# Optimization experiments

Hardware: AMD Instinct MI355X
Metric: run time of the kernel (lower is better)

## Reference

```python
import jax, jax.numpy as jnp
import numpy as np

B, T, I, H, O = 256, 512, 64, 512, 1


def _lstm_layer(x, Wih, Whh, bih, bhh):
    # x: [B, T, in]; Wih: [4H, in]; Whh: [4H, H]
    # Precompute input contribution for all timesteps (big GEMM, no recurrence).
    xg = jnp.einsum('bti,gi->btg', x, Wih) + bih + bhh  # [B, T, 4H]
    h0 = jnp.zeros((x.shape[0], Whh.shape[1]), x.dtype)
    c0 = jnp.zeros_like(h0)

    def step(carry, xt):
        h, c = carry
        gates = xt + h @ Whh.T  # [B, 4H]
        i, f, g, o = jnp.split(gates, 4, axis=-1)  # PyTorch gate order i,f,g,o
        i = jax.nn.sigmoid(i)
        f = jax.nn.sigmoid(f)
        g = jnp.tanh(g)
        o = jax.nn.sigmoid(o)
        c = f * c + i * g
        h = o * jnp.tanh(c)
        return (h, c), h

    _, hs = jax.lax.scan(step, (h0, c0), jnp.swapaxes(xg, 0, 1))  # [T, B, H]
    return jnp.swapaxes(hs, 0, 1)  # [B, T, H]


def setup_inputs() -> dict:
    key = jax.random.key(0)
    ks = jax.random.split(key, 12)
    s = 1.0 / np.sqrt(H)
    u = lambda k, shp: jax.random.uniform(k, shp, jnp.float32, -s, s)
    return {
        'x': jax.random.normal(ks[0], (B, T, I), jnp.float32),
        'Wih0': u(ks[1], (4 * H, I)),
        'Whh0': u(ks[2], (4 * H, H)),
        'bih0': u(ks[3], (4 * H,)),
        'bhh0': u(ks[4], (4 * H,)),
        'Wih1': u(ks[5], (4 * H, H)),
        'Whh1': u(ks[6], (4 * H, H)),
        'bih1': u(ks[7], (4 * H,)),
        'bhh1': u(ks[8], (4 * H,)),
        'Wfc': u(ks[9], (O, H)),
        'bfc': u(ks[10], (O,)),
    }


def reference(x, Wih0, Whh0, bih0, bhh0, Wih1, Whh1, bih1, bhh1, Wfc, bfc):
    h1 = _lstm_layer(x, Wih0, Whh0, bih0, bhh0)   # [B, T, H]
    h2 = _lstm_layer(h1, Wih1, Whh1, bih1, bhh1)  # [B, T, H]
    return h2[:, -1] @ Wfc.T + bfc  # [B, O]
```

## Files before the change

kernel.cpp:

```cpp
#include <hip/hip_runtime.h>

typedef unsigned short u16;
typedef unsigned long long u64;
typedef short bf16x8 __attribute__((ext_vector_type(8)));
typedef float f32x4 __attribute__((ext_vector_type(4)));

#define B_ 256
#define T_ 512
#define I_ 64
#define H_ 512
#define RING 32

#define OFF_F0    0u
#define OFF_F1    32768u
#define OFF_F2    65536u
#define OFF_F3    98304u
#define OFF_B0    131072u
#define OFF_B1    139264u
#define OFF_WIH0  147456u
#define OFF_WHH0  409600u
#define OFF_WIH1  2506752u
#define OFF_WHH1  4603904u
#define OFF_HX1   6701056u
#define OFF_H1R   7225344u
#define WS_NEEDED 15613952u

#define AQ __ATOMIC_RELAXED
#define SC __HIP_MEMORY_SCOPE_AGENT

static __device__ __forceinline__ u16 f2b(float f) {
  union { float f; unsigned u; } v; v.f = f;
  unsigned r = (v.u + 0x7FFFu + ((v.u >> 16) & 1u)) >> 16;
  return (u16)r;
}
static __device__ __forceinline__ float sigm(float x) { return 1.f / (1.f + __expf(-x)); }
static __device__ __forceinline__ float tanh_(float x) { return 1.f - 2.f / (__expf(2.f * x) + 1.f); }

__global__ void prep_kernel(const float* __restrict__ Wih0, const float* __restrict__ Whh0,
                            const float* __restrict__ bih0, const float* __restrict__ bhh0,
                            const float* __restrict__ Wih1, const float* __restrict__ Whh1,
                            const float* __restrict__ bih1, const float* __restrict__ bhh1,
                            const float* __restrict__ bfc, float* __restrict__ out,
                            char* __restrict__ ws) {
  unsigned* flags = (unsigned*)(ws + OFF_F0);
  float* b0 = (float*)(ws + OFF_B0);
  float* b1 = (float*)(ws + OFF_B1);
  u16* wih0b = (u16*)(ws + OFF_WIH0);
  u16* whh0b = (u16*)(ws + OFF_WHH0);
  u16* wih1b = (u16*)(ws + OFF_WIH1);
  u16* whh1b = (u16*)(ws + OFF_WHH1);

  long long i = (long long)blockIdx.x * 256 + threadIdx.x;
  if (i < 32768) { __hip_atomic_store(&flags[i], 0u, AQ, SC); return; }
  i -= 32768;
  if (i < 256) { out[i] = bfc[0]; return; }
  i -= 256;
  if (i < 2048) { b0[i] = bih0[i] + bhh0[i]; return; }
  i -= 2048;
  if (i < 2048) { b1[i] = bih1[i] + bhh1[i]; return; }
  i -= 2048;
  if (i < 131072) { wih0b[i] = f2b(Wih0[i]); return; }
  i -= 131072;
  if (i < 1048576) { whh0b[i] = f2b(Whh0[i]); return; }
  i -= 1048576;
  if (i < 1048576) { wih1b[i] = f2b(Wih1[i]); return; }
  i -= 1048576;
  if (i < 1048576) { whh1b[i] = f2b(Whh1[i]); return; }
}

template <bool IS_L0>
__device__ __forceinline__ void lstm_body(
    int bx,
    const float* __restrict__ x,
    const u16* __restrict__ Wib,
    const u16* __restrict__ Whb,
    const float* __restrict__ bias,
    unsigned* __restrict__ hx32,
    u16* __restrict__ h1ring,
    const float* __restrict__ Wfc, float* __restrict__ out,
    unsigned* __restrict__ fR,
    unsigned* __restrict__ fP,
    unsigned* __restrict__ fC,
    float* __restrict__ Gp_s)
{
  const int tid = threadIdx.x;
  const int wv = tid >> 6;
  const int lane = tid & 63;
  const int quad = lane >> 4;
  const int l15 = lane & 15;
  const int jn = bx & 31;
  const int ib = bx >> 5;

  bf16x8 Bh[4][4];
#pragma unroll
  for (int r = 0; r < 4; ++r)
#pragma unroll
    for (int nt = 0; nt < 4; ++nt)
      Bh[r][nt] = *(const bf16x8*)&Whb[(size_t)(nt * 512 + jn * 16 + l15) * 512 +
                                       (wv * 4 + r) * 32 + quad * 8];
  bf16x8 Bx[4][4];
  bf16x8 Bx0[4];
  if constexpr (IS_L0) {
    if (wv < 2) {
#pragma unroll
      for (int nt = 0; nt < 4; ++nt)
        Bx0[nt] = *(const bf16x8*)&Wib[(size_t)(nt * 512 + jn * 16 + l15) * 64 +
                                       wv * 32 + quad * 8];
    }
  } else {
#pragma unroll
    for (int r = 0; r < 4; ++r)
#pragma unroll
      for (int nt = 0; nt < 4; ++nt)
        Bx[r][nt] = *(const bf16x8*)&Wib[(size_t)(nt * 512 + jn * 16 + l15) * 512 +
                                         (wv * 4 + r) * 32 + quad * 8];
  }

  const int erow = tid >> 3;
  const int ecp = tid & 7;
  float bias2[4][2];
#pragma unroll
  for (int g = 0; g < 4; ++g) {
    bias2[g][0] = bias[g * 512 + jn * 16 + 2 * ecp];
    bias2[g][1] = bias[g * 512 + jn * 16 + 2 * ecp + 1];
  }
  float cst2[2] = {0.f, 0.f};
  const f32x4 zf = {0.f, 0.f, 0.f, 0.f};
  const unsigned lineoff = ((unsigned)ib * 32 + jn) * 32;

  const int bg = ib * 32 + erow;
  const int hg = jn * 16 + 2 * ecp;
  const unsigned stoff = (unsigned)(((hg >> 3) * 256 + bg) * 4 + (ecp & 3));

  for (int t = 0; t < T_; ++t) {
    f32x4 acc[2][4];
#pragma unroll
    for (int mt = 0; mt < 2; ++mt)
#pragma unroll
      for (int nt = 0; nt < 4; ++nt) acc[mt][nt] = zf;

    if constexpr (IS_L0) {
      if (wv < 2) {
        const float* xp = x + ((size_t)(ib * 32 + l15) * T_ + t) * 64 + wv * 32 + quad * 8;
        const float* xq = xp + (size_t)16 * T_ * 64;
        float4 xa = *(const float4*)xp;
        float4 xb = *(const float4*)(xp + 4);
        float4 xc = *(const float4*)xq;
        float4 xd = *(const float4*)(xq + 4);
        union { unsigned u[4]; bf16x8 v; } P0, P1;
        P0.u[0] = (unsigned)f2b(xa.x) | ((unsigned)f2b(xa.y) << 16);
        P0.u[1] = (unsigned)f2b(xa.z) | ((unsigned)f2b(xa.w) << 16);
        P0.u[2] = (unsigned)f2b(xb.x) | ((unsigned)f2b(xb.y) << 16);
        P0.u[3] = (unsigned)f2b(xb.z) | ((unsigned)f2b(xb.w) << 16);
        P1.u[0] = (unsigned)f2b(xc.x) | ((unsigned)f2b(xc.y) << 16);
        P1.u[1] = (unsigned)f2b(xc.z) | ((unsigned)f2b(xc.w) << 16);
        P1.u[2] = (unsigned)f2b(xd.x) | ((unsigned)f2b(xd.y) << 16);
        P1.u[3] = (unsigned)f2b(xd.z) | ((unsigned)f2b(xd.w) << 16);
#pragma unroll
        for (int nt = 0; nt < 4; ++nt) {
          acc[0][nt] = __builtin_amdgcn_mfma_f32_16x16x32_bf16(P0.v, Bx0[nt], acc[0][nt], 0, 0, 0);
          acc[1][nt] = __builtin_amdgcn_mfma_f32_16x16x32_bf16(P1.v, Bx0[nt], acc[1][nt], 0, 0, 0);
        }
      }
      if (t && wv == 0) {
        unsigned tgtR = (unsigned)t;
        unsigned tgtC = (t >= RING) ? (unsigned)(t - RING + 1) : 0u;
        for (;;) {
          unsigned vv, tg;
          if (lane < 32) { vv = __hip_atomic_load(&fR[lineoff + lane], AQ, SC); tg = tgtR; }
          else           { vv = __hip_atomic_load(&fC[lineoff + lane - 32], AQ, SC); tg = tgtC; }
          if (!__any(vv < tg)) break;
        }
      }
      __syncthreads();
    } else {
      if (wv == 0) {
        unsigned tgtP = (unsigned)(t + 1);
        unsigned tgtR = (unsigned)t;
        for (;;) {
          unsigned vv, tg;
          if (lane < 32) { vv = __hip_atomic_load(&fP[lineoff + lane], AQ, SC); tg = tgtP; }
          else           { vv = __hip_atomic_load(&fR[lineoff + lane - 32], AQ, SC); tg = tgtR; }
          if (!__any(vv < tg)) break;
        }
      }
      __syncthreads();
      const u64* hq1 = (const u64*)h1ring + (size_t)(t & (RING - 1)) * (B_ * H_ / 4);
#pragma unroll
      for (int r = 0; r < 4; ++r) {
        int ks = wv * 4 + r;
        bf16x8 af[2];
#pragma unroll
        for (int mt = 0; mt < 2; ++mt) {
          const u64* p = hq1 + (size_t)((ks * 4 + quad) * 256 + ib * 32 + mt * 16 + l15) * 2;
          union { u64 q[2]; bf16x8 v; } u;
          u.q[0] = __hip_atomic_load(p, AQ, SC);
          u.q[1] = __hip_atomic_load(p + 1, AQ, SC);
          af[mt] = u.v;
        }
#pragma unroll
        for (int nt = 0; nt < 4; ++nt) {
          acc[0][nt] = __builtin_amdgcn_mfma_f32_16x16x32_bf16(af[0], Bx[r][nt], acc[0][nt], 0, 0, 0);
          acc[1][nt] = __builtin_amdgcn_mfma_f32_16x16x32_bf16(af[1], Bx[r][nt], acc[1][nt], 0, 0, 0);
        }
      }
    }

    if (t) {
      const u64* hq;
      if constexpr (IS_L0)
        hq = (const u64*)h1ring + (size_t)((t - 1) & (RING - 1)) * (B_ * H_ / 4);
      else
        hq = (const u64*)hx32 + (size_t)(t & 1) * (B_ * H_ / 4);
      bf16x8 af[4][2];
#pragma unroll
      for (int r = 0; r < 4; ++r) {
        int ks = wv * 4 + r;
#pragma unroll
        for (int mt = 0; mt < 2; ++mt) {
          const u64* p = hq + (size_t)((ks * 4 + quad) * 256 + ib * 32 + mt * 16 + l15) * 2;
          union { u64 q[2]; bf16x8 v; } u;
          u.q[0] = __hip_atomic_load(p, AQ, SC);
          u.q[1] = __hip_atomic_load(p + 1, AQ, SC);
          af[r][mt] = u.v;
        }
      }
#pragma unroll
      for (int r = 0; r < 4; ++r)
#pragma unroll
        for (int mt = 0; mt < 2; ++mt)
#pragma unroll
          for (int nt = 0; nt < 4; ++nt)
            acc[mt][nt] = __builtin_amdgcn_mfma_f32_16x16x32_bf16(af[r][mt], Bh[r][nt],
                                                                  acc[mt][nt], 0, 0, 0);
    }

#pragma unroll
    for (int mt = 0; mt < 2; ++mt)
#pragma unroll
      for (int nt = 0; nt < 4; ++nt)
#pragma unroll
        for (int rr = 0; rr < 4; ++rr)
          Gp_s[(wv * 32 + mt * 16 + quad * 4 + rr) * 68 + nt * 16 + l15] = acc[mt][nt][rr];
    __syncthreads();

    {
      float pre[4][2];
#pragma unroll
      for (int g = 0; g < 4; ++g) {
        int c = g * 16 + 2 * ecp;
        float s0 = bias2[g][0], s1 = bias2[g][1];
#pragma unroll
        for (int w = 0; w < 4; ++w) {
          s0 += Gp_s[(w * 32 + erow) * 68 + c];
          s1 += Gp_s[(w * 32 + erow) * 68 + c + 1];
        }
        pre[g][0] = s0; pre[g][1] = s1;
      }
      float hv[2];
#pragma unroll
      for (int j = 0; j < 2; ++j) {
        float iv = sigm(pre[0][j]);
        float fv = sigm(pre[1][j]);
        float gv = tanh_(pre[2][j]);
        float ov = sigm(pre[3][j]);
        float cn = fv * cst2[j] + iv * gv;
        cst2[j] = cn;
        hv[j] = ov * tanh_(cn);
      }
      unsigned pack = (unsigned)f2b(hv[0]) | ((unsigned)f2b(hv[1]) << 16);
      if constexpr (IS_L0) {
        unsigned* ring32 = (unsigned*)h1ring;
        __hip_atomic_store(&ring32[(size_t)(t & (RING - 1)) * (B_ * H_ / 2) + stoff],
                           pack, AQ, SC);
      } else {
        __hip_atomic_store(&hx32[(size_t)((t + 1) & 1) * (B_ * H_ / 2) + stoff], pack, AQ, SC);
        if (t == T_ - 1) {
          float part = hv[0] * Wfc[hg] + hv[1] * Wfc[hg + 1];
          part += __shfl_down(part, 4, 8);
          part += __shfl_down(part, 2, 8);
          part += __shfl_down(part, 1, 8);
          if (ecp == 0) atomicAdd(&out[bg], part);
        }
      }
    }

    __syncthreads();
    if (wv == 0) {
      unsigned val = (unsigned)(t + 1);
      if constexpr (IS_L0) {
        if (lane < 32) {
          if (t + 1 < T_)
            __hip_atomic_store(&fR[((unsigned)ib * 32 + lane) * 32 + jn], val, AQ, SC);
        } else {
          __hip_atomic_store(&fP[((unsigned)ib * 32 + (lane - 32)) * 32 + jn], val, AQ, SC);
        }
      } else {
        if (t + 1 < T_) {
          if (lane < 32)
            __hip_atomic_store(&fR[((unsigned)ib * 32 + lane) * 32 + jn], val, AQ, SC);
          else
            __hip_atomic_store(&fC[((unsigned)ib * 32 + (lane - 32)) * 32 + jn], val, AQ, SC);
        }
      }
    }
  }
}

__global__ __launch_bounds__(256, 2) void lstm_fused(
    const float* __restrict__ x,
    const u16* __restrict__ wih0, const u16* __restrict__ whh0, const float* __restrict__ b0,
    const u16* __restrict__ wih1, const u16* __restrict__ whh1, const float* __restrict__ b1,
    unsigned* __restrict__ hx1, u16* __restrict__ h1ring,
    const float* __restrict__ Wfc, float* __restrict__ out,
    unsigned* __restrict__ f0, unsigned* __restrict__ f1, unsigned* __restrict__ f2,
    unsigned* __restrict__ f3)
{
  __shared__ __align__(16) float Gp_s[4 * 32 * 68];
  if (blockIdx.x < 256)
    lstm_body<true>(blockIdx.x, x, wih0, whh0, b0, (unsigned*)nullptr, h1ring,
                    (const float*)nullptr, (float*)nullptr, f0, f1, f3, Gp_s);
  else
    lstm_body<false>(blockIdx.x - 256, (const float*)nullptr, wih1, whh1, b1, hx1, h1ring,
                     Wfc, out, f2, f1, f3, Gp_s);
}

extern "C" void kernel_launch(void* const* d_in, const int* in_sizes, int n_in,
                              void* d_out, int out_size, void* d_ws, size_t ws_size,
                              hipStream_t stream) {
  if (ws_size < (size_t)WS_NEEDED) return;

  const float* x    = (const float*)d_in[0];
  const float* Wih0 = (const float*)d_in[1];
  const float* Whh0 = (const float*)d_in[2];
  const float* bih0 = (const float*)d_in[3];
  const float* bhh0 = (const float*)d_in[4];
  const float* Wih1 = (const float*)d_in[5];
  const float* Whh1 = (const float*)d_in[6];
  const float* bih1 = (const float*)d_in[7];
  const float* bhh1 = (const float*)d_in[8];
  const float* Wfc  = (const float*)d_in[9];
  const float* bfc  = (const float*)d_in[10];

  char* ws = (char*)d_ws;
  unsigned* f0   = (unsigned*)(ws + OFF_F0);
  unsigned* f1   = (unsigned*)(ws + OFF_F1);
  unsigned* f2   = (unsigned*)(ws + OFF_F2);
  unsigned* f3   = (unsigned*)(ws + OFF_F3);
  float* b0      = (float*)(ws + OFF_B0);
  float* b1      = (float*)(ws + OFF_B1);
  u16* wih0b     = (u16*)(ws + OFF_WIH0);
  u16* whh0b     = (u16*)(ws + OFF_WHH0);
  u16* wih1b     = (u16*)(ws + OFF_WIH1);
  u16* whh1b     = (u16*)(ws + OFF_WHH1);
  unsigned* hx1  = (unsigned*)(ws + OFF_HX1);
  u16* h1ring    = (u16*)(ws + OFF_H1R);
  float* out     = (float*)d_out;

  prep_kernel<<<12948, 256, 0, stream>>>(Wih0, Whh0, bih0, bhh0, Wih1, Whh1, bih1, bhh1,
                                         bfc, out, ws);

  lstm_fused<<<512, 256, 0, stream>>>(x, wih0b, whh0b, b0, wih1b, whh1b, b1,
                                      hx1, h1ring, Wfc, out, f0, f1, f2, f3);
}
```

Baseline: 2.848 ms.

## Prefetch layer-0 flag wait in layer-1, double-load spin polls, transpose gate scratch

Layer 1 now waits for layer-0 progress one step ahead, checking that h1 for step t+1 is ready, and does this after its input-projection MFMAs instead of before them, so the ring read overlaps the flag wait. The spin loop keeps two outstanding atomic loads in flight per iteration to shorten poll latency. Wave priority is raised around the recurrent MFMA and gate section. The LDS scratch for partial gates is transposed so accumulators are stored as vector f32x4 writes. The ring read in layer 1 now happens before the flag check for that step, which relies on the initial wait and the one-step-ahead wait having covered it. Final flag stores are no longer skipped on the last step.

```diff
diff --git a/kernel.cpp b/kernel.cpp
--- a/kernel.cpp
+++ b/kernel.cpp
@@ -35,6 +35,16 @@
 }
 static __device__ __forceinline__ float sigm(float x) { return 1.f / (1.f + __expf(-x)); }
 static __device__ __forceinline__ float tanh_(float x) { return 1.f - 2.f / (__expf(2.f * x) + 1.f); }
+
+static __device__ __forceinline__ void spin2(const unsigned* __restrict__ pa, unsigned tg) {
+  unsigned a = __hip_atomic_load(pa, AQ, SC);
+  for (;;) {
+    unsigned b = __hip_atomic_load(pa, AQ, SC);
+    if (!__any(a < tg)) break;
+    a = __hip_atomic_load(pa, AQ, SC);
+    if (!__any(b < tg)) break;
+  }
+}
 
 __global__ void prep_kernel(const float* __restrict__ Wih0, const float* __restrict__ Whh0,
                             const float* __restrict__ bih0, const float* __restrict__ bhh0,
@@ -132,6 +142,17 @@
   const int hg = jn * 16 + 2 * ecp;
   const unsigned stoff = (unsigned)(((hg >> 3) * 256 + bg) * 4 + (ecp & 3));
 
+  const unsigned* pollP;
+  if constexpr (IS_L0)
+    pollP = (lane < 32) ? &fR[lineoff + lane] : &fC[lineoff + (lane - 32)];
+  else
+    pollP = (lane < 32) ? &fR[lineoff + lane] : &fP[lineoff + (lane - 32)];
+
+  if constexpr (!IS_L0) {
+    if (wv == 0) spin2(&fP[lineoff + (lane & 31)], 1u);
+    __syncthreads();
+  }
+
   for (int t = 0; t < T_; ++t) {
     f32x4 acc[2][4];
 #pragma unroll
@@ -163,28 +184,12 @@
         }
       }
       if (t && wv == 0) {
-        unsigned tgtR = (unsigned)t;
-        unsigned tgtC = (t >= RING) ? (unsigned)(t - RING + 1) : 0u;
-        for (;;) {
-          unsigned vv, tg;
-          if (lane < 32) { vv = __hip_atomic_load(&fR[lineoff + lane], AQ, SC); tg = tgtR; }
-          else           { vv = __hip_atomic_load(&fC[lineoff + lane - 32], AQ, SC); tg = tgtC; }
-          if (!__any(vv < tg)) break;
-        }
+        const unsigned tg = (lane < 32) ? (unsigned)t
+                            : ((t >= RING) ? (unsigned)(t - RING + 1) : 0u);
+        spin2(pollP, tg);
       }
       __syncthreads();
     } else {
-      if (wv == 0) {
-        unsigned tgtP = (unsigned)(t + 1);
-        unsigned tgtR = (unsigned)t;
-        for (;;) {
-          unsigned vv, tg;
-          if (lane < 32) { vv = __hip_atomic_load(&fP[lineoff + lane], AQ, SC); tg = tgtP; }
-          else           { vv = __hip_atomic_load(&fR[lineoff + lane - 32], AQ, SC); tg = tgtR; }
-          if (!__any(vv < tg)) break;
-        }
-      }
-      __syncthreads();
       const u64* hq1 = (const u64*)h1ring + (size_t)(t & (RING - 1)) * (B_ * H_ / 4);
 #pragma unroll
       for (int r = 0; r < 4; ++r) {
@@ -204,7 +209,15 @@
           acc[1][nt] = __builtin_amdgcn_mfma_f32_16x16x32_bf16(af[1], Bx[r][nt], acc[1][nt], 0, 0, 0);
         }
       }
-    }
+      if (wv == 0) {
+        unsigned tP = (unsigned)(t + 2); if (tP > (unsigned)T_) tP = (unsigned)T_;
+        const unsigned tg = (lane < 32) ? (unsigned)t : tP;
+        spin2(pollP, tg);
+      }
+      __syncthreads();
+    }
+
+    __builtin_amdgcn_s_setprio(1);
 
     if (t) {
       const u64* hq;
@@ -239,23 +252,21 @@
     for (int mt = 0; mt < 2; ++mt)
 #pragma unroll
       for (int nt = 0; nt < 4; ++nt)
-#pragma unroll
-        for (int rr = 0; rr < 4; ++rr)
-          Gp_s[(wv * 32 + mt * 16 + quad * 4 + rr) * 68 + nt * 16 + l15] = acc[mt][nt][rr];
+        *(f32x4*)&Gp_s[(nt * 16 + l15) * 132 + wv * 32 + mt * 16 + quad * 4] = acc[mt][nt];
     __syncthreads();
 
     {
       float pre[4][2];
 #pragma unroll
       for (int g = 0; g < 4; ++g) {
-        int c = g * 16 + 2 * ecp;
-        float s0 = bias2[g][0], s1 = bias2[g][1];
-#pragma unroll
-        for (int w = 0; w < 4; ++w) {
-          s0 += Gp_s[(w * 32 + erow) * 68 + c];
-          s1 += Gp_s[(w * 32 + erow) * 68 + c + 1];
-        }
-        pre[g][0] = s0; pre[g][1] = s1;
+#pragma unroll
+        for (int j = 0; j < 2; ++j) {
+          const int c = g * 16 + 2 * ecp + j;
+          float s = bias2[g][j];
+#pragma unroll
+          for (int w = 0; w < 4; ++w) s += Gp_s[c * 132 + w * 32 + erow];
+          pre[g][j] = s;
+        }
       }
       float hv[2];
 #pragma unroll
@@ -284,24 +295,21 @@
         }
       }
     }
+    __builtin_amdgcn_s_setprio(0);
 
     __syncthreads();
     if (wv == 0) {
       unsigned val = (unsigned)(t + 1);
       if constexpr (IS_L0) {
-        if (lane < 32) {
-          if (t + 1 < T_)
-            __hip_atomic_store(&fR[((unsigned)ib * 32 + lane) * 32 + jn], val, AQ, SC);
-        } else {
+        if (lane < 32)
+          __hip_atomic_store(&fR[((unsigned)ib * 32 + lane) * 32 + jn], val, AQ, SC);
+        else
           __hip_atomic_store(&fP[((unsigned)ib * 32 + (lane - 32)) * 32 + jn], val, AQ, SC);
-        }
       } else {
-        if (t + 1 < T_) {
-          if (lane < 32)
-            __hip_atomic_store(&fR[((unsigned)ib * 32 + lane) * 32 + jn], val, AQ, SC);
-          else
-            __hip_atomic_store(&fC[((unsigned)ib * 32 + (lane - 32)) * 32 + jn], val, AQ, SC);
-        }
+        if (lane < 32)
+          __hip_atomic_store(&fR[((unsigned)ib * 32 + lane) * 32 + jn], val, AQ, SC);
+        else
+          __hip_atomic_store(&fC[((unsigned)ib * 32 + (lane - 32)) * 32 + jn], val, AQ, SC);
       }
     }
   }
@@ -316,7 +324,7 @@
     unsigned* __restrict__ f0, unsigned* __restrict__ f1, unsigned* __restrict__ f2,
     unsigned* __restrict__ f3)
 {
-  __shared__ __align__(16) float Gp_s[4 * 32 * 68];
+  __shared__ __align__(16) float Gp_s[64 * 132];
   if (blockIdx.x < 256)
     lstm_body<true>(blockIdx.x, x, wih0, whh0, b0, (unsigned*)nullptr, h1ring,
                     (const float*)nullptr, (float*)nullptr, f0, f1, f3, Gp_s);
```

Result: faster. 2.497 ms (-12.4%).
